# Performance work log

Measured on AMD Instinct MI355X. Metric: run time of the kernel, lower is better.

The kernel has to match this reference:

```python
import jax, jax.numpy as jnp
import numpy as np

TEMP = 1.0
EPS = 1e-8
DIM = 1024
CODEBOOK_SIZE = 8192
N = 8192


def setup_inputs() -> dict:
    key = jax.random.key(0)
    k_h, k_cb, k_w, k_b = jax.random.split(key, 4)
    h = jax.random.normal(k_h, (N, DIM), dtype=jnp.float32)
    codebook = jax.random.normal(k_cb, (CODEBOOK_SIZE, DIM), dtype=jnp.float32)
    # RMSNorm scale initialized to ones (as in the torch module)
    scale = jnp.ones((DIM,), dtype=jnp.float32)
    # nn.Linear(dim, dim): weight [out, in], bias [out]
    bound = 1.0 / np.sqrt(DIM)
    W = jax.random.uniform(k_w, (DIM, DIM), dtype=jnp.float32, minval=-bound, maxval=bound)
    b = jax.random.uniform(k_b, (DIM,), dtype=jnp.float32, minval=-bound, maxval=bound)
    return {"h": h, "codebook": codebook, "scale": scale, "W": W, "b": b}


def reference(h, codebook, scale, W, b):
    # Squared distances via GEMM identity: ||h-c||^2 = ||h||^2 + ||c||^2 - 2 h.c
    h_sq = jnp.sum(h * h, axis=-1, keepdims=True)              # [N, 1]
    c_sq = jnp.sum(codebook * codebook, axis=-1)               # [K]
    dist = h_sq + c_sq[None, :] - 2.0 * (h @ codebook.T)       # [N, K]
    q = jax.nn.softmax(-dist / TEMP, axis=-1)                  # [N, K]
    z_e = q @ codebook                                         # [N, D]
    # residual MLP: RMSNorm then Linear
    r = h - z_e
    rms = jnp.sqrt(jnp.mean(r * r, axis=-1, keepdims=True))
    x = r / (rms + EPS) * scale
    z_q = z_e + x @ W.T + b
    return z_q
```

## Files before the change

### kernel.cpp

```cpp
#include <hip/hip_runtime.h>

typedef unsigned short u16;
typedef unsigned char u8;
typedef signed char s8;
typedef __attribute__((ext_vector_type(8))) short bf16x8;
typedef __attribute__((ext_vector_type(4))) float f32x4;
typedef __attribute__((ext_vector_type(4))) int i32x4;
typedef __attribute__((ext_vector_type(16))) int i32x16;

__device__ __forceinline__ u16 f2bf(float x) {
  unsigned int u = __float_as_uint(x);
  u = u + 0x7FFFu + ((u >> 16) & 1u);
  return (u16)(u >> 16);
}
__device__ __forceinline__ float bf2f(u16 v) {
  return __uint_as_float(((unsigned int)v) << 16);
}

typedef const __attribute__((address_space(1))) void gas_void;
typedef __attribute__((address_space(3))) void las_void;

__device__ __forceinline__ void gld_lds16(const void* g, void* l) {
  __builtin_amdgcn_global_load_lds((gas_void*)g, (las_void*)l, 16, 0, 0);
}

#define CAP 512
#define DU8 8

__global__ __launch_bounds__(256) void gemm_c8(
    const s8* __restrict__ A0, const s8* __restrict__ B0,
    u8* __restrict__ S, const float* __restrict__ c_sq) {
  __shared__ __align__(16) s8 lA[128 * 128];
  __shared__ __align__(16) s8 lB[128 * 128];
  int tid = threadIdx.x, wave = tid >> 6, lane = tid & 63;
  long bm = (long)blockIdx.y * 128, bn = (long)blockIdx.x * 128;
  int wm = (wave >> 1) * 64, wn = (wave & 1) * 64;
  int l31 = lane & 31, kg = lane >> 5;
  int srow = wave * 8 + (lane >> 3);

  i32x16 acc[2][2];
#pragma unroll
  for (int i = 0; i < 2; ++i)
#pragma unroll
    for (int j = 0; j < 2; ++j)
#pragma unroll
      for (int r = 0; r < 16; ++r) acc[i][j][r] = 0;

  const s8* ap = A0 + bm * 1024;
  const s8* bp = B0 + bn * 1024;

  for (int k0 = 0; k0 < 1024; k0 += 128) {
    __syncthreads();
#pragma unroll
    for (int c = 0; c < 4; ++c) {
      int sc2 = ((lane & 7) ^ (lane >> 3) ^ ((c * 4 + wave) & 7)) * 16;
      long go = (long)(c * 32 + srow) * 1024 + k0 + sc2;
      int ldoff = c * 4096 + wave * 1024;
      gld_lds16(ap + go, lA + ldoff);
      gld_lds16(bp + go, lB + ldoff);
    }
    __syncthreads();
#pragma unroll
    for (int kk = 0; kk < 4; ++kk) {
      i32x4 af[2], bf[2];
#pragma unroll
      for (int i = 0; i < 2; ++i) {
        int ra = wm + i * 32 + l31;
        int rxa = (ra & 7) ^ ((ra >> 3) & 7);
        af[i] = *(const i32x4*)&lA[ra * 128 + ((kk * 2 + kg) ^ rxa) * 16];
        int rb = wn + i * 32 + l31;
        int rxb = (rb & 7) ^ ((rb >> 3) & 7);
        bf[i] = *(const i32x4*)&lB[rb * 128 + ((kk * 2 + kg) ^ rxb) * 16];
      }
#pragma unroll
      for (int i = 0; i < 2; ++i)
#pragma unroll
        for (int j = 0; j < 2; ++j)
          acc[i][j] = __builtin_amdgcn_mfma_i32_32x32x32_i8(af[i], bf[j], acc[i][j], 0, 0, 0);
    }
  }

#pragma unroll
  for (int i = 0; i < 2; ++i) {
#pragma unroll
    for (int j = 0; j < 2; ++j) {
      long cg = bn + wn + j * 32 + l31;
      float csq = c_sq[cg];
#pragma unroll
      for (int r = 0; r < 16; ++r) {
        long rg = bm + wm + i * 32 + (r & 3) + 8 * (r >> 2) + 4 * kg;
        float v = csq - (float)acc[i][j][r] * 0.0078125f;
        int q = (int)rintf((v - 1024.f) * 0.25f) + 128;
        q = q < 0 ? 0 : (q > 255 ? 255 : q);
        S[rg * 8192 + cg] = (u8)q;
      }
    }
  }
}

__global__ __launch_bounds__(256) void gemm_zq(
    const u16* __restrict__ A0, long lda,
    const u16* __restrict__ B0, long ldb,
    float* __restrict__ C, long ldc, int K,
    const u16* __restrict__ aux0, const float* __restrict__ aux1) {
  __shared__ __align__(16) u16 lA0[128 * 64];
  __shared__ __align__(16) u16 lB0[64 * 64];

  int tid = threadIdx.x;
  int wave = tid >> 6, lane = tid & 63;
  long bm = (long)blockIdx.y * 128, bn = (long)blockIdx.x * 64;
  int wm = (wave >> 1) * 64, wn = (wave & 1) * 32;
  int r15 = lane & 15, kg = lane >> 4;
  int srow = wave * 8 + (lane >> 3);
  int scol = ((lane & 7) ^ (lane >> 3)) * 8;

  f32x4 acc[4][2];
#pragma unroll
  for (int i = 0; i < 4; ++i)
#pragma unroll
    for (int j = 0; j < 2; ++j) acc[i][j] = (f32x4){0.f, 0.f, 0.f, 0.f};

  for (int k0 = 0; k0 < K; k0 += 64) {
    __syncthreads();
#pragma unroll
    for (int c = 0; c < 4; ++c) {
      const u16* g = A0 + (bm + c * 32 + srow) * lda + k0 + scol;
      gld_lds16(g, lA0 + c * 2048 + wave * 512);
    }
#pragma unroll
    for (int c = 0; c < 2; ++c) {
      const u16* g = B0 + (bn + c * 32 + srow) * ldb + k0 + scol;
      gld_lds16(g, lB0 + c * 2048 + wave * 512);
    }
    __syncthreads();

#pragma unroll
    for (int kk = 0; kk < 2; ++kk) {
      int cu = ((kk * 4 + kg) ^ (r15 & 7)) * 8;
      bf16x8 bh[2];
#pragma unroll
      for (int j = 0; j < 2; ++j)
        bh[j] = *(const bf16x8*)&lB0[(wn + j * 16 + r15) * 64 + cu];
#pragma unroll
      for (int i = 0; i < 4; ++i) {
        bf16x8 ah = *(const bf16x8*)&lA0[(wm + i * 16 + r15) * 64 + cu];
#pragma unroll
        for (int j = 0; j < 2; ++j)
          acc[i][j] = __builtin_amdgcn_mfma_f32_16x16x32_bf16(ah, bh[j], acc[i][j], 0, 0, 0);
      }
    }
  }

#pragma unroll
  for (int i = 0; i < 4; ++i) {
    long rg = bm + wm + i * 16 + kg * 4;
#pragma unroll
    for (int j = 0; j < 2; ++j) {
      long cg = bn + wn + j * 16 + r15;
      f32x4 v = acc[i][j];
      float bb = aux1[cg];
#pragma unroll
      for (int r = 0; r < 4; ++r)
        C[(rg + r) * ldc + cg] = v[r] + bf2f(aux0[(rg + r) * ldc + cg]) + bb;
    }
  }
}

__device__ __forceinline__ int q8(float x) {
  float q = rintf(x * 16.f);
  q = fminf(fmaxf(q, -127.f), 127.f);
  return (int)q;
}

__global__ __launch_bounds__(256) void prep_h_w(const float* __restrict__ h,
                                                s8* __restrict__ q0,
                                                const float* __restrict__ W,
                                                u16* __restrict__ Wbf) {
  int b = blockIdx.x;
  if (b < 8192) {
    int i = b * 256 + threadIdx.x;
    float4 v = ((const float4*)h)[i];
    unsigned int w = (unsigned int)((q8(v.x) & 0xFF) | ((q8(v.y) & 0xFF) << 8) |
                                    ((q8(v.z) & 0xFF) << 16) | ((q8(v.w) & 0xFF) << 24));
    ((unsigned int*)q0)[i] = w;
  } else {
    int i = (b - 8192) * 256 + threadIdx.x;
    float4 v = ((const float4*)W)[i];
    ushort4 o;
    o.x = f2bf(v.x); o.y = f2bf(v.y); o.z = f2bf(v.z); o.w = f2bf(v.w);
    ((ushort4*)Wbf)[i] = o;
  }
}

__global__ __launch_bounds__(256) void prep_cb_i8(const float* __restrict__ cb,
                                                  s8* __restrict__ q0,
                                                  float* __restrict__ c_sq) {
  long k = blockIdx.x;
  int t = threadIdx.x, lane = t & 63, wave = t >> 6;
  float4 v = ((const float4*)(cb + k * 1024))[t];
  unsigned int w = (unsigned int)((q8(v.x) & 0xFF) | ((q8(v.y) & 0xFF) << 8) |
                                  ((q8(v.z) & 0xFF) << 16) | ((q8(v.w) & 0xFF) << 24));
  ((unsigned int*)(q0 + k * 1024))[t] = w;
  float ss = v.x * v.x + v.y * v.y + v.z * v.z + v.w * v.w;
#pragma unroll
  for (int o = 32; o; o >>= 1) ss += __shfl_xor(ss, o);
  __shared__ float sc[4];
  if (lane == 0) sc[wave] = ss;
  __syncthreads();
  if (t == 0) c_sq[k] = sc[0] + sc[1] + sc[2] + sc[3];
}

__global__ __launch_bounds__(256) void refine_rms(
    const float* __restrict__ h, const float* __restrict__ cb,
    const float* __restrict__ csq, const u8* __restrict__ Sq,
    const float* __restrict__ scale,
    u16* __restrict__ z_e, u16* __restrict__ x) {
  long m = blockIdx.x;
  int t = threadIdx.x, lane = t & 63, wave = t >> 6;
  __shared__ int cand[CAP];
  __shared__ int smi[4], wsum[4], ncand;
  __shared__ float smf[4], ssum[4], sc[4];
  __shared__ float lacc[4][1024];

  const uint4* row4 = (const uint4*)(Sq + m * 8192);
  uint4 va = row4[t], vb = row4[256 + t];
  unsigned int w[8] = {va.x, va.y, va.z, va.w, vb.x, vb.y, vb.z, vb.w};
  int bmin = 255;
#pragma unroll
  for (int i = 0; i < 8; ++i)
#pragma unroll
    for (int j = 0; j < 4; ++j) {
      int b = (w[i] >> (8 * j)) & 0xFF;
      bmin = b < bmin ? b : bmin;
    }
#pragma unroll
  for (int o = 32; o; o >>= 1) {
    int y = __shfl_xor(bmin, o);
    bmin = y < bmin ? y : bmin;
  }
  if (lane == 0) smi[wave] = bmin;
  __syncthreads();
  bmin = min(min(smi[0], smi[1]), min(smi[2], smi[3]));
  int thr = bmin + DU8;
  int c = 0;
#pragma unroll
  for (int i = 0; i < 8; ++i)
#pragma unroll
    for (int j = 0; j < 4; ++j)
      c += (((w[i] >> (8 * j)) & 0xFF) <= (unsigned)thr);
  int pre = c;
#pragma unroll
  for (int o = 1; o < 64; o <<= 1) {
    int y = __shfl_up(pre, o);
    if (lane >= o) pre += y;
  }
  if (lane == 63) wsum[wave] = pre;
  __syncthreads();
  int base = 0;
#pragma unroll
  for (int wv = 0; wv < 4; ++wv) base += (wv < wave) ? wsum[wv] : 0;
  int pos = base + pre - c;
#pragma unroll
  for (int i = 0; i < 8; ++i)
#pragma unroll
    for (int j = 0; j < 4; ++j) {
      int b = (w[i] >> (8 * j)) & 0xFF;
      if (b <= thr) {
        int col = (i < 4 ? t * 16 : 4096 + t * 16) + (i & 3) * 4 + j;
        if (pos < CAP) cand[pos] = col;
        ++pos;
      }
    }
  if (t == 0) {
    int tot = wsum[0] + wsum[1] + wsum[2] + wsum[3];
    ncand = tot < CAP ? tot : CAP;
  }
  __syncthreads();
  int n = ncand;

  const float4* h4 = (const float4*)(h + m * 1024);
  float4 hw[4];
#pragma unroll
  for (int i = 0; i < 4; ++i) hw[i] = h4[lane * 4 + i];

  float mw = -3.0e38f, sw = 0.f;
  float4 a0 = {0.f, 0.f, 0.f, 0.f}, a1 = a0, a2 = a0, a3 = a0;
  for (int j = wave; j < n; j += 4) {
    long k = cand[j];
    const float4* c4 = (const float4*)(cb + k * 1024);
    float4 cv0 = c4[lane * 4 + 0], cv1 = c4[lane * 4 + 1];
    float4 cv2 = c4[lane * 4 + 2], cv3 = c4[lane * 4 + 3];
    float d = hw[0].x * cv0.x + hw[0].y * cv0.y + hw[0].z * cv0.z + hw[0].w * cv0.w +
              hw[1].x * cv1.x + hw[1].y * cv1.y + hw[1].z * cv1.z + hw[1].w * cv1.w +
              hw[2].x * cv2.x + hw[2].y * cv2.y + hw[2].z * cv2.z + hw[2].w * cv2.w +
              hw[3].x * cv3.x + hw[3].y * cv3.y + hw[3].z * cv3.z + hw[3].w * cv3.w;
#pragma unroll
    for (int o = 32; o; o >>= 1) d += __shfl_xor(d, o);
    float lg = 2.f * d - csq[k];
    if (lg > mw) {
      float r = __expf(mw - lg);
      sw *= r;
      a0.x *= r; a0.y *= r; a0.z *= r; a0.w *= r;
      a1.x *= r; a1.y *= r; a1.z *= r; a1.w *= r;
      a2.x *= r; a2.y *= r; a2.z *= r; a2.w *= r;
      a3.x *= r; a3.y *= r; a3.z *= r; a3.w *= r;
      mw = lg;
    }
    float wgt = __expf(lg - mw);
    sw += wgt;
    a0.x += wgt * cv0.x; a0.y += wgt * cv0.y; a0.z += wgt * cv0.z; a0.w += wgt * cv0.w;
    a1.x += wgt * cv1.x; a1.y += wgt * cv1.y; a1.z += wgt * cv1.z; a1.w += wgt * cv1.w;
    a2.x += wgt * cv2.x; a2.y += wgt * cv2.y; a2.z += wgt * cv2.z; a2.w += wgt * cv2.w;
    a3.x += wgt * cv3.x; a3.y += wgt * cv3.y; a3.z += wgt * cv3.z; a3.w += wgt * cv3.w;
  }
  if (lane == 0) { smf[wave] = mw; ssum[wave] = sw; }
  __syncthreads();
  float M = fmaxf(fmaxf(smf[0], smf[1]), fmaxf(smf[2], smf[3]));
  float Stot = ssum[0] * __expf(smf[0] - M) + ssum[1] * __expf(smf[1] - M) +
               ssum[2] * __expf(smf[2] - M) + ssum[3] * __expf(smf[3] - M);
  float rw = __expf(mw - M);
  float* lw = &lacc[wave][lane * 16];
  *(float4*)(lw + 0) = (float4){a0.x * rw, a0.y * rw, a0.z * rw, a0.w * rw};
  *(float4*)(lw + 4) = (float4){a1.x * rw, a1.y * rw, a1.z * rw, a1.w * rw};
  *(float4*)(lw + 8) = (float4){a2.x * rw, a2.y * rw, a2.z * rw, a2.w * rw};
  *(float4*)(lw + 12) = (float4){a3.x * rw, a3.y * rw, a3.z * rw, a3.w * rw};
  __syncthreads();
  float rs = 1.f / Stot;
  float4 p0 = *(const float4*)&lacc[0][t * 4];
  float4 p1 = *(const float4*)&lacc[1][t * 4];
  float4 p2 = *(const float4*)&lacc[2][t * 4];
  float4 p3 = *(const float4*)&lacc[3][t * 4];
  float4 ze;
  ze.x = (p0.x + p1.x + p2.x + p3.x) * rs;
  ze.y = (p0.y + p1.y + p2.y + p3.y) * rs;
  ze.z = (p0.z + p1.z + p2.z + p3.z) * rs;
  ze.w = (p0.w + p1.w + p2.w + p3.w) * rs;
  ushort4 zo;
  zo.x = f2bf(ze.x); zo.y = f2bf(ze.y); zo.z = f2bf(ze.z); zo.w = f2bf(ze.w);
  *(ushort4*)(z_e + m * 1024 + t * 4) = zo;
  float4 hv = h4[t];
  float4 r;
  r.x = hv.x - ze.x; r.y = hv.y - ze.y; r.z = hv.z - ze.z; r.w = hv.w - ze.w;
  float ss = r.x * r.x + r.y * r.y + r.z * r.z + r.w * r.w;
#pragma unroll
  for (int o = 32; o; o >>= 1) ss += __shfl_xor(ss, o);
  if (lane == 0) sc[wave] = ss;
  __syncthreads();
  float tot = sc[0] + sc[1] + sc[2] + sc[3];
  float inv = 1.f / (sqrtf(tot * (1.f / 1024.f)) + 1e-8f);
  float4 s4 = ((const float4*)scale)[t];
  ushort4 o;
  o.x = f2bf(r.x * inv * s4.x); o.y = f2bf(r.y * inv * s4.y);
  o.z = f2bf(r.z * inv * s4.z); o.w = f2bf(r.w * inv * s4.w);
  *(ushort4*)(x + m * 1024 + t * 4) = o;
}

extern "C" void kernel_launch(void* const* d_in, const int* in_sizes, int n_in,
                              void* d_out, int out_size, void* d_ws, size_t ws_size,
                              hipStream_t stream) {
  const float* h = (const float*)d_in[0];
  const float* cb = (const float*)d_in[1];
  const float* scale = (const float*)d_in[2];
  const float* W = (const float*)d_in[3];
  const float* b = (const float*)d_in[4];
  float* out = (float*)d_out;

  char* ws = (char*)d_ws;
  size_t off = 0;
  auto alloc = [&](size_t bytes) -> char* {
    char* p = ws + off;
    off = (off + bytes + 255) & ~(size_t)255;
    return p;
  };
  s8* h8 = (s8*)alloc(8192L * 1024);
  s8* c8 = (s8*)alloc(8192L * 1024);
  u16* Wbf = (u16*)alloc(1024L * 1024 * 2);
  float* c_sq = (float*)alloc(8192L * 4);
  u16* z_e = (u16*)alloc(8192L * 1024 * 2);
  u16* x = (u16*)alloc(8192L * 1024 * 2);
  u8* Sq = (u8*)alloc(8192L * 8192);

  prep_h_w<<<9216, 256, 0, stream>>>(h, h8, W, Wbf);
  prep_cb_i8<<<8192, 256, 0, stream>>>(cb, c8, c_sq);

  gemm_c8<<<dim3(64, 64), 256, 0, stream>>>(h8, c8, Sq, c_sq);
  refine_rms<<<8192, 256, 0, stream>>>(h, cb, c_sq, Sq, scale, z_e, x);
  gemm_zq<<<dim3(16, 64), 256, 0, stream>>>(x, 1024L, Wbf, 1024L,
                                            out, 1024L, 1024, z_e, b);
}
```

Baseline: 182.5 us.

## Double-buffer int8 distance GEMM K-loop and use nontemporal score stores/loads

The int8 distance GEMM now stages 64-wide K slices into two LDS buffers, so the next slice's global-to-LDS copy is issued while MFMAs run on the current one. The XOR swizzle is reworked for the narrower rows, and one barrier per iteration replaces two. The quantized score matrix is written and later read with nontemporal hints to keep the large one-shot buffer from polluting the caches. The trade-off is twice as many loop iterations with smaller tiles per step, plus possible LDS bank-conflict changes from the new swizzle.

```diff
diff --git a/kernel.cpp b/kernel.cpp
--- a/kernel.cpp
+++ b/kernel.cpp
@@ -7,6 +7,7 @@
 typedef __attribute__((ext_vector_type(4))) float f32x4;
 typedef __attribute__((ext_vector_type(4))) int i32x4;
 typedef __attribute__((ext_vector_type(16))) int i32x16;
+typedef __attribute__((ext_vector_type(4))) unsigned int u32x4;
 
 __device__ __forceinline__ u16 f2bf(float x) {
   unsigned int u = __float_as_uint(x);
@@ -30,13 +31,14 @@
 __global__ __launch_bounds__(256) void gemm_c8(
     const s8* __restrict__ A0, const s8* __restrict__ B0,
     u8* __restrict__ S, const float* __restrict__ c_sq) {
-  __shared__ __align__(16) s8 lA[128 * 128];
-  __shared__ __align__(16) s8 lB[128 * 128];
+  __shared__ __align__(16) s8 lA[2][128 * 64];
+  __shared__ __align__(16) s8 lB[2][128 * 64];
   int tid = threadIdx.x, wave = tid >> 6, lane = tid & 63;
   long bm = (long)blockIdx.y * 128, bn = (long)blockIdx.x * 128;
   int wm = (wave >> 1) * 64, wn = (wave & 1) * 64;
   int l31 = lane & 31, kg = lane >> 5;
-  int srow = wave * 8 + (lane >> 3);
+  int srow = lane >> 2;
+  int scol = ((lane & 3) ^ ((lane >> 2) & 3) ^ ((lane >> 4) & 3)) * 16;
 
   i32x16 acc[2][2];
 #pragma unroll
@@ -49,28 +51,36 @@
   const s8* ap = A0 + bm * 1024;
   const s8* bp = B0 + bn * 1024;
 
-  for (int k0 = 0; k0 < 1024; k0 += 128) {
-    __syncthreads();
-#pragma unroll
-    for (int c = 0; c < 4; ++c) {
-      int sc2 = ((lane & 7) ^ (lane >> 3) ^ ((c * 4 + wave) & 7)) * 16;
-      long go = (long)(c * 32 + srow) * 1024 + k0 + sc2;
-      int ldoff = c * 4096 + wave * 1024;
-      gld_lds16(ap + go, lA + ldoff);
-      gld_lds16(bp + go, lB + ldoff);
-    }
-    __syncthreads();
-#pragma unroll
-    for (int kk = 0; kk < 4; ++kk) {
+  auto STAGE = [&](int buf, int k0) {
+#pragma unroll
+    for (int rr = 0; rr < 2; ++rr) {
+      long row = rr * 64 + wave * 16 + srow;
+      long go = row * 1024 + k0 + scol;
+      int ldoff = rr * 4096 + wave * 1024;
+      gld_lds16(ap + go, lA[buf] + ldoff);
+      gld_lds16(bp + go, lB[buf] + ldoff);
+    }
+  };
+
+  STAGE(0, 0);
+  __syncthreads();
+  int cur = 0;
+  for (int k0 = 0; k0 < 1024; k0 += 64) {
+    if (k0 < 960) STAGE(cur ^ 1, k0 + 64);
+    const s8* la = lA[cur];
+    const s8* lb = lB[cur];
+#pragma unroll
+    for (int kk = 0; kk < 2; ++kk) {
+      int ks = kk * 2 + kg;
       i32x4 af[2], bf[2];
 #pragma unroll
       for (int i = 0; i < 2; ++i) {
         int ra = wm + i * 32 + l31;
-        int rxa = (ra & 7) ^ ((ra >> 3) & 7);
-        af[i] = *(const i32x4*)&lA[ra * 128 + ((kk * 2 + kg) ^ rxa) * 16];
+        int sa = ks ^ (ra & 3) ^ ((ra >> 2) & 3);
+        af[i] = *(const i32x4*)&la[ra * 64 + sa * 16];
         int rb = wn + i * 32 + l31;
-        int rxb = (rb & 7) ^ ((rb >> 3) & 7);
-        bf[i] = *(const i32x4*)&lB[rb * 128 + ((kk * 2 + kg) ^ rxb) * 16];
+        int sb = ks ^ (rb & 3) ^ ((rb >> 2) & 3);
+        bf[i] = *(const i32x4*)&lb[rb * 64 + sb * 16];
       }
 #pragma unroll
       for (int i = 0; i < 2; ++i)
@@ -78,6 +88,8 @@
         for (int j = 0; j < 2; ++j)
           acc[i][j] = __builtin_amdgcn_mfma_i32_32x32x32_i8(af[i], bf[j], acc[i][j], 0, 0, 0);
     }
+    __syncthreads();
+    cur ^= 1;
   }
 
 #pragma unroll
@@ -92,7 +104,7 @@
         float v = csq - (float)acc[i][j][r] * 0.0078125f;
         int q = (int)rintf((v - 1024.f) * 0.25f) + 128;
         q = q < 0 ? 0 : (q > 255 ? 255 : q);
-        S[rg * 8192 + cg] = (u8)q;
+        __builtin_nontemporal_store((u8)q, &S[rg * 8192 + cg]);
       }
     }
   }
@@ -222,8 +234,9 @@
   __shared__ float smf[4], ssum[4], sc[4];
   __shared__ float lacc[4][1024];
 
-  const uint4* row4 = (const uint4*)(Sq + m * 8192);
-  uint4 va = row4[t], vb = row4[256 + t];
+  const u32x4* row4 = (const u32x4*)(Sq + m * 8192);
+  u32x4 va = __builtin_nontemporal_load(&row4[t]);
+  u32x4 vb = __builtin_nontemporal_load(&row4[256 + t]);
   unsigned int w[8] = {va.x, va.y, va.z, va.w, vb.x, vb.y, vb.z, vb.w};
   int bmin = 255;
 #pragma unroll
```

After: 206.1 us. 1.13x slower.
